# Optimization experiments

Hardware: AMD Instinct MI355X
Metric: run time of the kernel (lower is better)

## Reference

```python
import jax, jax.numpy as jnp
import numpy as np

N_NODES = 100000
N_EDGES = 1600000
DIM_IN, DIM_H, DIM_OUT = 500, 64, 8


def setup_inputs() -> dict:
    key = jax.random.key(0)
    k_x, k_e, k_w1, k_w2 = jax.random.split(key, 4)
    x = jax.random.normal(k_x, (N_NODES, DIM_IN), dtype=jnp.float32)
    edge_index = jax.random.randint(k_e, (2, N_EDGES), 0, N_NODES, dtype=jnp.int32)
    # Glorot-ish init for linear weights, zero bias (PyG GCNConv default)
    W1 = jax.random.normal(k_w1, (DIM_IN, DIM_H), dtype=jnp.float32) * (1.0 / np.sqrt(DIM_IN))
    b1 = jnp.zeros((DIM_H,), dtype=jnp.float32)
    W2 = jax.random.normal(k_w2, (DIM_H, DIM_OUT), dtype=jnp.float32) * (1.0 / np.sqrt(DIM_H))
    b2 = jnp.zeros((DIM_OUT,), dtype=jnp.float32)
    return {"x": x, "edge_index": edge_index, "W1": W1, "b1": b1, "W2": W2, "b2": b2}


def _gcn_conv(h, W, b, src, dst, edge_norm, num_nodes):
    """GCNConv: out = D^{-1/2}(A+I)D^{-1/2} (h W) + b, via gather/scatter over edges."""
    hw = h @ W                                  # [N, d_out] dense transform
    msg = hw[src] * edge_norm[:, None]          # [E+N, d_out] gather + scale
    agg = jax.ops.segment_sum(msg, dst, num_segments=num_nodes)  # scatter-add
    return agg + b


def reference(x, edge_index, W1, b1, W2, b2):
    num_nodes = x.shape[0]
    # Add self-loops (PyG GCNConv default: add_self_loops=True)
    loops = jnp.arange(num_nodes, dtype=edge_index.dtype)
    src = jnp.concatenate([edge_index[0], loops])
    dst = jnp.concatenate([edge_index[1], loops])
    # Symmetric normalization from in-degree of loop-augmented graph
    deg = jax.ops.segment_sum(jnp.ones_like(dst, dtype=x.dtype), dst,
                              num_segments=num_nodes)
    dinv = jnp.where(deg > 0, jax.lax.rsqrt(deg), 0.0)
    edge_norm = dinv[src] * dinv[dst]           # [E+N]
    # Eval-mode forward (dropout is identity when not training)
    h = jax.nn.relu(_gcn_conv(x, W1, b1, src, dst, edge_norm, num_nodes))
    h = _gcn_conv(h, W2, b2, src, dst, edge_norm, num_nodes)
    return jax.nn.log_softmax(h, axis=1)
```

## Files before the change

### kernel.cpp

```cpp
#include <hip/hip_runtime.h>
#include <stdint.h>

#define NN 100000
#define NE 1600000
#define DIN 500
#define DH 64
#define DOUT 8
#define KP 512
#define MAXDEG 64
#define LDSW 132

typedef __attribute__((ext_vector_type(8))) short short8;
typedef __attribute__((ext_vector_type(4))) float f32x4;
typedef unsigned short ushort_t;

static __device__ __forceinline__ ushort_t f2bf(float f) {
  union { float f; uint32_t u; } v; v.f = f;
  uint32_t u = v.u;
  return (ushort_t)((u + 0x7FFFu + ((u >> 16) & 1u)) >> 16);
}
static __device__ __forceinline__ float bf2f(ushort_t h) {
  union { uint32_t u; float f; } v; v.u = ((uint32_t)h) << 16;
  return v.f;
}

__global__ __launch_bounds__(256) void k_fill(const int* __restrict__ ei,
                                              int* __restrict__ cursor,
                                              int* __restrict__ colsrc) {
  int id = blockIdx.x * 256 + threadIdx.x;
  if (id >= NE + NN) return;
  int s, d;
  if (id < NE) { s = ei[id]; d = ei[NE + id]; }
  else { s = id - NE; d = s; }
  int pos = atomicAdd(&cursor[d], 1);
  if (pos < MAXDEG) colsrc[d * MAXDEG + pos] = s;
}

__global__ __launch_bounds__(256) void k_dinv(const int* __restrict__ cursor,
                                              float* __restrict__ dinv) {
  int v = blockIdx.x * 256 + threadIdx.x;
  if (v >= NN) return;
  dinv[v] = 1.0f / sqrtf((float)cursor[v]);
}

__global__ __launch_bounds__(256) void k_w1cvt(const float* __restrict__ W1,
                                               ushort_t* __restrict__ bh,
                                               ushort_t* __restrict__ bl) {
  int id = blockIdx.x * 256 + threadIdx.x;
  if (id >= DH * KP) return;
  int i = id & 7, lane = (id >> 3) & 63, off = (id >> 9) & 3, kkg = id >> 11;
  int r = lane & 15, g = lane >> 4;
  int col = off * 16 + r;
  int k = kkg * 32 + g * 8 + i;
  float v = (k < DIN) ? W1[k * DH + col] : 0.0f;
  ushort_t hi = f2bf(v);
  bh[id] = hi;
  bl[id] = f2bf(v - bf2f(hi));
}

__global__ __launch_bounds__(256) void k_gemm1(const float* __restrict__ x,
                                               const ushort_t* __restrict__ bh,
                                               const ushort_t* __restrict__ bl,
                                               ushort_t* __restrict__ hwb) {
  __shared__ float lds[64 * LDSW];
  int tid = threadIdx.x;
  int lane = tid & 63, w = tid >> 6;
  int r = lane & 15, g = lane >> 4;
  int row0 = blockIdx.x * 64;

  f32x4 acc0 = {0,0,0,0}, acc1 = {0,0,0,0}, acc2 = {0,0,0,0}, acc3 = {0,0,0,0};

  for (int ch = 0; ch < 4; ++ch) {
    __syncthreads();
#pragma unroll
    for (int j = 0; j < 8; ++j) {
      int idx = j * 256 + tid;
      int lr = idx >> 5;
      int pos = idx & 31;
      int kq = ch * 32 + pos;
      float4 val = {0, 0, 0, 0};
      int grow = row0 + lr;
      if (kq < 125 && grow < NN)
        val = *(const float4*)(x + (size_t)grow * DIN + kq * 4);
      *(float4*)(&lds[lr * LDSW + pos * 4]) = val;
    }
    __syncthreads();
#pragma unroll
    for (int kk = 0; kk < 4; ++kk) {
      int kb = kk * 32 + g * 8;
      const float* lp = &lds[(w * 16 + r) * LDSW + kb];
      float4 v0 = *(const float4*)lp;
      float4 v1 = *(const float4*)(lp + 4);
      float a[8] = {v0.x, v0.y, v0.z, v0.w, v1.x, v1.y, v1.z, v1.w};
      short8 ah, al;
#pragma unroll
      for (int i = 0; i < 8; ++i) {
        ushort_t hi = f2bf(a[i]);
        ah[i] = (short)hi;
        al[i] = (short)f2bf(a[i] - bf2f(hi));
      }
      int kkg = ch * 4 + kk;
      const ushort_t* bph = bh + (size_t)(kkg * 4) * 512 + lane * 8;
      const ushort_t* bpl = bl + (size_t)(kkg * 4) * 512 + lane * 8;
#define TILE(T, OFF)                                                            \
      {                                                                         \
        short8 bhf = *(const short8*)(bph + (OFF) * 512);                       \
        short8 blf = *(const short8*)(bpl + (OFF) * 512);                       \
        T = __builtin_amdgcn_mfma_f32_16x16x32_bf16(ah, bhf, T, 0, 0, 0);       \
        T = __builtin_amdgcn_mfma_f32_16x16x32_bf16(al, bhf, T, 0, 0, 0);       \
        T = __builtin_amdgcn_mfma_f32_16x16x32_bf16(ah, blf, T, 0, 0, 0);       \
      }
      TILE(acc0, 0) TILE(acc1, 1) TILE(acc2, 2) TILE(acc3, 3)
#undef TILE
    }
  }
  int wrow0 = row0 + w * 16;
#pragma unroll
  for (int i = 0; i < 4; ++i) {
    int orow = wrow0 + g * 4 + i;
    if (orow < NN) {
      ushort_t* o = hwb + (size_t)orow * DH + r;
      o[0]  = f2bf(acc0[i]);
      o[16] = f2bf(acc1[i]);
      o[32] = f2bf(acc2[i]);
      o[48] = f2bf(acc3[i]);
    }
  }
}

__global__ __launch_bounds__(256) void k_agg1(const ushort_t* __restrict__ hwb,
                                              const int* __restrict__ colsrc,
                                              const int* __restrict__ cnt,
                                              const float* __restrict__ dinv,
                                              const float* __restrict__ b1,
                                              const float* __restrict__ W2,
                                              float* __restrict__ hw2) {
  int lane = threadIdx.x & 63;
  int v = blockIdx.x * 4 + (threadIdx.x >> 6);
  if (v >= NN) return;
  int c = cnt[v]; if (c > MAXDEG) c = MAXDEG;
  float dv = dinv[v];
  const int* cl = colsrc + v * MAXDEG;
  int si = cl[lane];
  bool act = lane < c;
  if (!act) si = 0;
  float nrmv = act ? dinv[si] * dv : 0.0f;
  float acc = 0.0f;
  for (int i0 = 0; i0 < c; i0 += 8) {
    float val[8];
#pragma unroll
    for (int j = 0; j < 8; ++j) {
      int s = __builtin_amdgcn_readlane(si, i0 + j);
      val[j] = bf2f(hwb[(size_t)s * DH + lane]);
    }
#pragma unroll
    for (int j = 0; j < 8; ++j) {
      float nrm = __uint_as_float(__builtin_amdgcn_readlane(__float_as_uint(nrmv), i0 + j));
      acc = fmaf(val[j], nrm, acc);
    }
  }
  float h = acc + b1[lane];
  h = h > 0.0f ? h : 0.0f;
  const float* w2r = W2 + lane * DOUT;
  float p0 = h * w2r[0], p1 = h * w2r[1], p2 = h * w2r[2], p3 = h * w2r[3];
  float p4 = h * w2r[4], p5 = h * w2r[5], p6 = h * w2r[6], p7 = h * w2r[7];
#pragma unroll
  for (int off = 32; off > 0; off >>= 1) {
    p0 += __shfl_xor(p0, off); p1 += __shfl_xor(p1, off);
    p2 += __shfl_xor(p2, off); p3 += __shfl_xor(p3, off);
    p4 += __shfl_xor(p4, off); p5 += __shfl_xor(p5, off);
    p6 += __shfl_xor(p6, off); p7 += __shfl_xor(p7, off);
  }
  if (lane == 0) {
    float4 q0 = {p0, p1, p2, p3}, q1 = {p4, p5, p6, p7};
    *(float4*)(hw2 + (size_t)v * DOUT)     = q0;
    *(float4*)(hw2 + (size_t)v * DOUT + 4) = q1;
  }
}

__global__ __launch_bounds__(256) void k_agg2(const float* __restrict__ hw2,
                                              const int* __restrict__ colsrc,
                                              const int* __restrict__ cnt,
                                              const float* __restrict__ dinv,
                                              const float* __restrict__ b2,
                                              float* __restrict__ out) {
  int lane = threadIdx.x & 63;
  int v = blockIdx.x * 4 + (threadIdx.x >> 6);
  if (v >= NN) return;
  int e = lane >> 3, f = lane & 7;
  int c = cnt[v]; if (c > MAXDEG) c = MAXDEG;
  float dv = dinv[v];
  const int* cl = colsrc + v * MAXDEG;
  float acc = 0.0f;
  for (int i0 = 0; i0 < c; i0 += 8) {
    int i = i0 + e;
    bool a2 = i < c;
    int s = a2 ? cl[i] : 0;
    float nrm = a2 ? dinv[s] * dv : 0.0f;
    float val = hw2[(size_t)s * DOUT + f] * nrm;
    val += __shfl_xor(val, 8);
    val += __shfl_xor(val, 16);
    val += __shfl_xor(val, 32);
    acc += val;
  }
  acc += b2[f];
  float m = acc;
  m = fmaxf(m, __shfl_xor(m, 1));
  m = fmaxf(m, __shfl_xor(m, 2));
  m = fmaxf(m, __shfl_xor(m, 4));
  float ex = expf(acc - m);
  float sum = ex;
  sum += __shfl_xor(sum, 1);
  sum += __shfl_xor(sum, 2);
  sum += __shfl_xor(sum, 4);
  float ls = m + logf(sum);
  if (e == 0) out[(size_t)v * DOUT + f] = acc - ls;
}

extern "C" void kernel_launch(void* const* d_in, const int* in_sizes, int n_in,
                              void* d_out, int out_size, void* d_ws, size_t ws_size,
                              hipStream_t stream) {
  const float* x  = (const float*)d_in[0];
  const int*   ei = (const int*)d_in[1];
  const float* W1 = (const float*)d_in[2];
  const float* b1 = (const float*)d_in[3];
  const float* W2 = (const float*)d_in[4];
  const float* b2 = (const float*)d_in[5];
  float* out = (float*)d_out;

  char* w = (char*)d_ws;
  size_t off = 0;
  auto alloc = [&](size_t bytes) {
    char* p = w + off;
    off += (bytes + 255) & ~(size_t)255;
    return (void*)p;
  };
  int*      cursor = (int*)alloc((size_t)NN * 4);
  float*    dinv   = (float*)alloc((size_t)NN * 4);
  ushort_t* bh     = (ushort_t*)alloc((size_t)DH * KP * 2);
  ushort_t* bl     = (ushort_t*)alloc((size_t)DH * KP * 2);
  int*      colsrc = (int*)alloc((size_t)NN * MAXDEG * 4);
  ushort_t* hwb    = (ushort_t*)alloc((size_t)NN * DH * 2);
  float*    hw2    = (float*)alloc((size_t)NN * DOUT * 4);

  hipMemsetAsync(cursor, 0, (size_t)NN * 4, stream);
  k_fill<<<(NE + NN + 255) / 256, 256, 0, stream>>>(ei, cursor, colsrc);
  k_dinv<<<(NN + 255) / 256, 256, 0, stream>>>(cursor, dinv);
  k_w1cvt<<<(DH * KP + 255) / 256, 256, 0, stream>>>(W1, bh, bl);
  k_gemm1<<<(NN + 63) / 64, 256, 0, stream>>>(x, bh, bl, hwb);
  k_agg1<<<(NN + 3) / 4, 256, 0, stream>>>(hwb, colsrc, cursor, dinv, b1, W2, hw2);
  k_agg2<<<(NN + 3) / 4, 256, 0, stream>>>(hw2, colsrc, cursor, dinv, b2, out);
}
```

Before: 317.6 us.

## Partition edge fill into destination-range passes to localize atomic scatter

Each thread in the CSR fill kernel now loads four edges, then makes 16 passes over destination-node ranges. In each pass it performs atomics and colsrc writes only for edges whose destination falls in the current range. The aim is to keep concurrent atomic and scatter traffic within a smaller address window, for better cache and TLB locality on cursor and colsrc. In exchange, every thread runs 16 loop passes with branch checks, and pass-level concurrency may cost some parallelism.

```diff
diff --git a/kernel.cpp b/kernel.cpp
--- a/kernel.cpp
+++ b/kernel.cpp
@@ -10,6 +10,10 @@
 #define MAXDEG 64
 #define LDSW 132
 
+#define FILL_EPT 4
+#define FILL_PASSES 16
+#define FILL_RS ((NN + FILL_PASSES - 1) / FILL_PASSES)
+
 typedef __attribute__((ext_vector_type(8))) short short8;
 typedef __attribute__((ext_vector_type(4))) float f32x4;
 typedef unsigned short ushort_t;
@@ -27,13 +31,31 @@
 __global__ __launch_bounds__(256) void k_fill(const int* __restrict__ ei,
                                               int* __restrict__ cursor,
                                               int* __restrict__ colsrc) {
-  int id = blockIdx.x * 256 + threadIdx.x;
-  if (id >= NE + NN) return;
-  int s, d;
-  if (id < NE) { s = ei[id]; d = ei[NE + id]; }
-  else { s = id - NE; d = s; }
-  int pos = atomicAdd(&cursor[d], 1);
-  if (pos < MAXDEG) colsrc[d * MAXDEG + pos] = s;
+  int t = blockIdx.x * 256 + threadIdx.x;
+  const int T = gridDim.x * 256;
+  int s[FILL_EPT], d[FILL_EPT];
+#pragma unroll
+  for (int k = 0; k < FILL_EPT; ++k) {
+    int id = t + k * T;
+    s[k] = 0; d[k] = -1;
+    if (id < NE) { s[k] = ei[id]; d[k] = ei[NE + id]; }
+    else if (id < NE + NN) { s[k] = id - NE; d[k] = s[k]; }
+  }
+#pragma unroll 1
+  for (int p = 0; p < FILL_PASSES; ++p) {
+    int lo = p * FILL_RS;
+    int hi = lo + FILL_RS;
+#pragma unroll
+    for (int k = 0; k < FILL_EPT; ++k) {
+      bool act = (d[k] >= lo) && (d[k] < hi);
+      if (__any(act)) {
+        if (act) {
+          int pos = atomicAdd(&cursor[d[k]], 1);
+          if (pos < MAXDEG) colsrc[d[k] * MAXDEG + pos] = s[k];
+        }
+      }
+    }
+  }
 }
 
 __global__ __launch_bounds__(256) void k_dinv(const int* __restrict__ cursor,
@@ -244,7 +266,8 @@
   float*    hw2    = (float*)alloc((size_t)NN * DOUT * 4);
 
   hipMemsetAsync(cursor, 0, (size_t)NN * 4, stream);
-  k_fill<<<(NE + NN + 255) / 256, 256, 0, stream>>>(ei, cursor, colsrc);
+  int fill_blocks = (NE + NN + 256 * FILL_EPT - 1) / (256 * FILL_EPT);
+  k_fill<<<fill_blocks, 256, 0, stream>>>(ei, cursor, colsrc);
   k_dinv<<<(NN + 255) / 256, 256, 0, stream>>>(cursor, dinv);
   k_w1cvt<<<(DH * KP + 255) / 256, 256, 0, stream>>>(W1, bh, bl);
   k_gemm1<<<(NN + 63) / 64, 256, 0, stream>>>(x, bh, bl, hwb);
```

Result: faster. 263.0 us (-17.2%).
